# Performance work log

Measured on AMD Instinct MI355X. Metric: run time of the kernel, lower is better.

Reference implementation:

```python
import jax, jax.numpy as jnp
import numpy as np

N = 50000      # nodes
E = 800000     # edges (avg degree 16)
IN, HID, OUT = 256, 128, 64
K, ALPHA = 4, 0.0  # APPNPConv(k=4, alpha=0.0)


def setup_inputs() -> dict:
    key = jax.random.key(0)
    ks = jax.random.split(key, 5)
    features = jax.random.normal(ks[0], (N, IN), jnp.float32)
    src = jax.random.randint(ks[1], (E,), 0, N, jnp.int32)
    dst = jax.random.randint(ks[2], (E,), 0, N, jnp.int32)
    W1 = jax.random.normal(ks[3], (IN, HID), jnp.float32) / np.float32(np.sqrt(IN))
    b1 = jnp.zeros((HID,), jnp.float32)
    W3 = jax.random.normal(ks[4], (HID, OUT), jnp.float32) / np.float32(np.sqrt(HID))
    b3 = jnp.zeros((OUT,), jnp.float32)
    return dict(features=features, src=src, dst=dst, W1=W1, b1=b1, W3=W3, b3=b3)


def _sym_norms(src, dst, n):
    # D_out^{-1/2} for source side, D_in^{-1/2} for destination side (DGL norm='both')
    ones = jnp.ones((src.shape[0],), jnp.float32)
    deg_out = jax.ops.segment_sum(ones, src, num_segments=n)
    deg_in = jax.ops.segment_sum(ones, dst, num_segments=n)
    return jnp.clip(deg_out, 1.0) ** -0.5, jnp.clip(deg_in, 1.0) ** -0.5


def _prop(x, src, dst, norm_src, norm_dst):
    # x: [N, D]. Symmetric-normalized SpMM: D_in^{-1/2} A D_out^{-1/2} x
    msg = (x * norm_src[:, None])[src]                       # [E, D] gather
    agg = jax.ops.segment_sum(msg, dst, num_segments=x.shape[0])  # [N, D] scatter-add
    return agg * norm_dst[:, None]


def reference(features, src, dst, W1, b1, W3, b3):
    ns, nd = _sym_norms(src, dst, N)
    # GraphConv 1 (weight-first since in_dim > hidden_dim; math identical either way)
    h = _prop(features @ W1, src, dst, ns, nd) + b1
    # dropout is identity in eval mode (training=False)
    # APPNPConv: k=4 power-iteration steps with teleport alpha=0.0
    h0 = h
    for _ in range(K):
        h = (1.0 - ALPHA) * _prop(h, src, dst, ns, nd) + ALPHA * h0
    # GraphConv 3
    out = _prop(h @ W3, src, dst, ns, nd) + b3
    return out
```

## Files before the change

### kernel.cpp

```cpp
#include <hip/hip_runtime.h>
#include <math.h>

#define N_NODES 50000
#define N_EDGES 800000
#define DIN 256
#define DHID 128
#define DOUT 64
#define CSTRIDE 64
#define ZROW N_NODES
#define HBLOCKS 256
#define HCHUNK (N_EDGES / HBLOCKS)
#define HWORDS (N_NODES / 4)
#define SLICE ((size_t)(N_NODES + 1) * 16)
#define NGROUPS (N_NODES / 4)
#define PBLOCKS 49

#define SB_SENT 3125
#define SB_HS (SB_SENT + HBLOCKS)
#define SB_HD (SB_HS + HBLOCKS)
#define SB_TOT (SB_HD + 66)

__global__ void k_setup(const int* __restrict__ src, const int* __restrict__ dst,
                        unsigned int* __restrict__ pS, unsigned int* __restrict__ pD,
                        unsigned int* __restrict__ csr32,
                        const float* __restrict__ W1, const float* __restrict__ b1,
                        const float* __restrict__ W3,
                        float* __restrict__ W13, float* __restrict__ bb,
                        float* __restrict__ Y0, float* __restrict__ Y1) {
    __shared__ unsigned int h[HWORDS];
    int bx = blockIdx.x, t = threadIdx.x;
    if (bx < SB_SENT) {
        unsigned int v = (unsigned int)ZROW | ((unsigned int)ZROW << 16);
        uint2 o; o.x = v; o.y = v;
        ((uint2*)csr32)[bx * 256 + t] = o;
        return;
    }
    if (bx < SB_HD) {
        const int* idx = (bx < SB_HS) ? src : dst;
        unsigned int* outp = (bx < SB_HS) ? pS : pD;
        int hb = bx - ((bx < SB_HS) ? SB_SENT : SB_HS);
        for (int w = t; w < HWORDS; w += 256) h[w] = 0u;
        __syncthreads();
        int base = hb * HCHUNK;
        for (int i = t; i < HCHUNK; i += 256) {
            int s = idx[base + i];
            atomicAdd(&h[s >> 2], 1u << ((s & 3) << 3));
        }
        __syncthreads();
        outp += (size_t)hb * HWORDS;
        for (int w = t; w < HWORDS; w += 256) outp[w] = h[w];
        return;
    }
    int vb = bx - SB_HD;
    if (vb == 65) {
        if (t < 64) {
            int qq = t >> 4, c2 = t & 15;
            Y0[(size_t)qq * SLICE + ((size_t)ZROW << 4) + c2] = 0.f;
            Y1[(size_t)qq * SLICE + ((size_t)ZROW << 4) + c2] = 0.f;
        }
        return;
    }
    if (vb == 64) {
        if (t < DOUT) {
            float s = 0.f;
            for (int k = 0; k < DHID; ++k) s += b1[k] * W3[k * DOUT + t];
            bb[t] = s;
        }
        return;
    }
    int idx2 = vb * 256 + t;
    int i = idx2 >> 6, j = idx2 & 63;
    float s = 0.f;
    for (int k = 0; k < DHID; ++k) s += W1[i * DHID + k] * W3[k * DOUT + j];
    W13[idx2] = s;
}

__global__ void k_hpre(const unsigned int* __restrict__ pS,
                       const unsigned int* __restrict__ pD,
                       unsigned int* __restrict__ prefix,
                       int* __restrict__ deg_in,
                       float* __restrict__ ns, float* __restrict__ nd,
                       float* __restrict__ cc, int* __restrict__ dparts) {
    __shared__ int lh[65];
    int t = threadIdx.x;
    if (t < 65) lh[t] = 0;
    __syncthreads();
    int wid = blockIdx.x * 256 + t;
    if (wid < HWORDS) {
        unsigned int o0 = 0, o1 = 0, o2 = 0, o3 = 0;
#pragma unroll 4
        for (int b = 0; b < HBLOCKS; ++b) {
            unsigned int w = pS[(size_t)b * HWORDS + wid];
            o0 += w & 0xffu; o1 += (w >> 8) & 0xffu;
            o2 += (w >> 16) & 0xffu; o3 += w >> 24;
        }
        unsigned int run = 0;
        for (int b = 0; b < HBLOCKS; ++b) {
            unsigned int w = pD[(size_t)b * HWORDS + wid];
            prefix[(size_t)b * HWORDS + wid] = run;
            run += w;
        }
        unsigned int i0 = run & 0xffu, i1 = (run >> 8) & 0xffu;
        unsigned int i2 = (run >> 16) & 0xffu, i3 = run >> 24;
        int4 di; di.x = (int)i0; di.y = (int)i1; di.z = (int)i2; di.w = (int)i3;
        *(int4*)(deg_in + (wid << 2)) = di;

        unsigned int dov[4] = {o0, o1, o2, o3};
        unsigned int div_[4] = {i0, i1, i2, i3};
        float4 vns, vnd, vcc;
        float* pns = &vns.x; float* pnd = &vnd.x; float* pcc = &vcc.x;
#pragma unroll
        for (int q = 0; q < 4; ++q) {
            int bin = (int)div_[q]; if (bin > 64) bin = 64;
            atomicAdd(&lh[bin], 1);
            unsigned int a = dov[q] < 1u ? 1u : dov[q];
            unsigned int b = div_[q] < 1u ? 1u : div_[q];
            float fa = 1.0f / sqrtf((float)a);
            float fb = 1.0f / sqrtf((float)b);
            pns[q] = fa; pnd[q] = fb; pcc[q] = fa * fb;
        }
        *(float4*)(ns + (wid << 2)) = vns;
        *(float4*)(nd + (wid << 2)) = vnd;
        *(float4*)(cc + (wid << 2)) = vcc;
    }
    __syncthreads();
    if (t < 65) dparts[blockIdx.x * 65 + t] = lh[t];
}

__global__ void k_dscan(const int* __restrict__ dparts, int* __restrict__ offs) {
    __shared__ int colsum[65], binbase[65];
    int t = threadIdx.x;
    if (t < 65) {
        int s = 0;
        for (int b = 0; b < PBLOCKS; ++b) s += dparts[b * 65 + t];
        colsum[t] = s;
    }
    __syncthreads();
    if (t == 0) {
        int run = 0;
        for (int k = 64; k >= 0; --k) { binbase[k] = run; run += colsum[k]; }
    }
    __syncthreads();
    if (t < 65) {
        int run = binbase[t];
        for (int b = 0; b < PBLOCKS; ++b) { offs[b * 65 + t] = run; run += dparts[b * 65 + t]; }
    }
}

__global__ void k_dscatter(const int* __restrict__ deg_in, const int* __restrict__ offs,
                           const float* __restrict__ cc, const float* __restrict__ ns,
                           const float* __restrict__ nd,
                           int* __restrict__ perm, int* __restrict__ inv,
                           int* __restrict__ degP, float* __restrict__ ccP,
                           float* __restrict__ nsP, float* __restrict__ ndP) {
    __shared__ int off[65];
    int t = threadIdx.x;
    if (t < 65) off[t] = offs[blockIdx.x * 65 + t];
    __syncthreads();
    int wid = blockIdx.x * 256 + t;
    if (wid < HWORDS) {
        int4 d4 = *(const int4*)(deg_in + (wid << 2));
        int dd[4] = {d4.x, d4.y, d4.z, d4.w};
#pragma unroll
        for (int k = 0; k < 4; ++k) {
            int node = (wid << 2) + k;
            int bin = dd[k] > 64 ? 64 : dd[k];
            int slot = atomicAdd(&off[bin], 1);
            perm[slot] = node; inv[node] = slot;
            degP[slot] = dd[k];
            ccP[slot] = cc[node]; nsP[slot] = ns[node]; ndP[slot] = nd[node];
        }
    }
}

__global__ void k_fill(const int* __restrict__ src, const int* __restrict__ dst,
                       const unsigned int* __restrict__ prefix,
                       const int* __restrict__ inv,
                       unsigned short* __restrict__ csr) {
    __shared__ unsigned int h[HWORDS];
    int t = threadIdx.x;
    const unsigned int* prow = prefix + (size_t)blockIdx.x * HWORDS;
    for (int w = t; w < HWORDS; w += 256) h[w] = prow[w];
    __syncthreads();
    int base = blockIdx.x * HCHUNK;
    for (int i = t; i < HCHUNK; i += 256) {
        int s = src[base + i], d = dst[base + i];
        int sh = (d & 3) << 3;
        unsigned int old = atomicAdd(&h[d >> 2], 1u << sh);
        int slot = (int)((old >> sh) & 0xffu);
        csr[((size_t)inv[d] << 6) + slot] = (unsigned short)inv[s];
    }
}

__global__ void k_gemm(const float* __restrict__ X, const float* __restrict__ W13,
                       const float* __restrict__ ns, const int* __restrict__ inv,
                       float* __restrict__ Y) {
    __shared__ float As[16][68];
    __shared__ float Bs[16][64];
    int tid = threadIdx.x;
    int tx = tid & 15, ty = tid >> 4;
    int row0 = blockIdx.x * 64;
    float acc[4][4];
#pragma unroll
    for (int i = 0; i < 4; ++i)
#pragma unroll
        for (int j = 0; j < 4; ++j) acc[i][j] = 0.f;

    int lr = tid >> 2;
    int lk = (tid & 3) << 2;
    int arow = row0 + lr;
    if (arow > N_NODES - 1) arow = N_NODES - 1;

    for (int k0 = 0; k0 < DIN; k0 += 16) {
        float4 a = *(const float4*)(X + (size_t)arow * DIN + k0 + lk);
        As[lk + 0][lr] = a.x; As[lk + 1][lr] = a.y;
        As[lk + 2][lr] = a.z; As[lk + 3][lr] = a.w;
        float4 b = *(const float4*)(W13 + (size_t)(k0 + (tid >> 4)) * DOUT + ((tid & 15) << 2));
        *(float4*)&Bs[tid >> 4][(tid & 15) << 2] = b;
        __syncthreads();
#pragma unroll
        for (int k = 0; k < 16; ++k) {
            float4 av = *(const float4*)&As[k][ty << 2];
            float4 bv = *(const float4*)&Bs[k][tx << 2];
            float ar[4] = {av.x, av.y, av.z, av.w};
            float br[4] = {bv.x, bv.y, bv.z, bv.w};
#pragma unroll
            for (int i = 0; i < 4; ++i)
#pragma unroll
                for (int j = 0; j < 4; ++j) acc[i][j] += ar[i] * br[j];
        }
        __syncthreads();
    }
    int qq = tx >> 2;
    int co = (tx & 3) << 2;
#pragma unroll
    for (int i = 0; i < 4; ++i) {
        int row = row0 + (ty << 2) + i;
        if (row < N_NODES) {
            float nsr = ns[row];
            int prow = inv[row];
            float4 o;
            o.x = acc[i][0] * nsr; o.y = acc[i][1] * nsr;
            o.z = acc[i][2] * nsr; o.w = acc[i][3] * nsr;
            *(float4*)(Y + (size_t)qq * SLICE + ((size_t)prow << 4) + co) = o;
        }
    }
}


template <int MODE>
__launch_bounds__(256, 8)
__global__ void k_spmm(const float* __restrict__ xs, float* __restrict__ ys,
                       const unsigned short* __restrict__ csr,
                       const int* __restrict__ degP,
                       const float* __restrict__ ccP, const float* __restrict__ nsP,
                       const float* __restrict__ ndP,
                       const float* __restrict__ bb, const float* __restrict__ b3,
                       const int* __restrict__ perm) {
    __shared__ unsigned short rows[4][4][64];
    int wid  = threadIdx.x >> 6;
    int lane = threadIdx.x & 63;
    int q    = (blockIdx.x & 7) >> 1;
    int half = blockIdx.x & 1;
    int g    = (blockIdx.x >> 3) * 8 + wid * 2 + half;
    if (g >= NGROUPS) return;
    int node0 = g << 2;

    int nn = lane >> 4, sl = lane & 15;
    const uint2* crow = (const uint2*)(csr + ((size_t)(node0 + nn) << 6)) + sl;
    uint2 rv = *crow;
    *(uint2*)(&rows[wid][nn][sl << 2]) = rv;

    int n0u = __builtin_amdgcn_readfirstlane(node0);
    int m = (degP[n0u] + 7) & ~7;

    int n = lane >> 4, e = (lane >> 2) & 3, c4 = lane & 3;
    const unsigned short* rd = &rows[wid][n][e];
    const float* xq = xs + (size_t)q * SLICE + (c4 << 2);

    float ax = 0.f, ay = 0.f, az = 0.f, aw = 0.f;
#define LDV(T) const float4 v##T = *(const float4*)(xq + ((size_t)rd[4 * (T)] << 4))
#define ACCV(T) ax += v##T.x; ay += v##T.y; az += v##T.z; aw += v##T.w
    if (m <= 8) {
        LDV(0); LDV(1);
        ACCV(0); ACCV(1);
    } else if (m <= 16) {
        LDV(0); LDV(1); LDV(2); LDV(3);
        ACCV(0); ACCV(1); ACCV(2); ACCV(3);
    } else if (m <= 24) {
        LDV(0); LDV(1); LDV(2); LDV(3); LDV(4); LDV(5);
        ACCV(0); ACCV(1); ACCV(2); ACCV(3); ACCV(4); ACCV(5);
    } else if (m <= 32) {
        LDV(0); LDV(1); LDV(2); LDV(3); LDV(4); LDV(5); LDV(6); LDV(7);
        ACCV(0); ACCV(1); ACCV(2); ACCV(3); ACCV(4); ACCV(5); ACCV(6); ACCV(7);
    } else {
        for (int j = 0; j < m; j += 8) {
            const float4 a = *(const float4*)(xq + ((size_t)rd[j] << 4));
            const float4 b = *(const float4*)(xq + ((size_t)rd[j + 4] << 4));
            ax += a.x; ay += a.y; az += a.z; aw += a.w;
            ax += b.x; ay += b.y; az += b.z; aw += b.w;
        }
    }
#undef LDV
#undef ACCV
    ax += __shfl_xor(ax, 4);  ay += __shfl_xor(ay, 4);
    az += __shfl_xor(az, 4);  aw += __shfl_xor(aw, 4);
    ax += __shfl_xor(ax, 8);  ay += __shfl_xor(ay, 8);
    az += __shfl_xor(az, 8);  aw += __shfl_xor(aw, 8);

    int nodeL = node0 + n;
    int colq  = (q << 4) + (c4 << 2);
    float4 r;
    if (MODE == 0) {
        float cv = ccP[nodeL], nv = nsP[nodeL];
        float4 bv = *(const float4*)(bb + colq);
        r.x = cv * ax + nv * bv.x; r.y = cv * ay + nv * bv.y;
        r.z = cv * az + nv * bv.z; r.w = cv * aw + nv * bv.w;
    } else if (MODE == 1) {
        float cv = ccP[nodeL];
        r.x = cv * ax; r.y = cv * ay; r.z = cv * az; r.w = cv * aw;
    } else {
        float dv = ndP[nodeL];
        float4 bv = *(const float4*)(b3 + colq);
        r.x = dv * ax + bv.x; r.y = dv * ay + bv.y;
        r.z = dv * az + bv.z; r.w = dv * aw + bv.w;
    }
    if (e == 0) {
        if (MODE == 2) {
            int orow = perm[nodeL];
            *(float4*)(ys + ((size_t)orow << 6) + colq) = r;
        } else {
            *(float4*)(ys + (size_t)q * SLICE + ((size_t)nodeL << 4) + (c4 << 2)) = r;
        }
    }
}


extern "C" void kernel_launch(void* const* d_in, const int* in_sizes, int n_in,
                              void* d_out, int out_size, void* d_ws, size_t ws_size,
                              hipStream_t stream) {
    const float* X   = (const float*)d_in[0];
    const int*   src = (const int*)d_in[1];
    const int*   dst = (const int*)d_in[2];
    const float* W1  = (const float*)d_in[3];
    const float* b1  = (const float*)d_in[4];
    const float* W3  = (const float*)d_in[5];
    const float* b3  = (const float*)d_in[6];
    float* out = (float*)d_out;

    char* ws = (char*)d_ws;
    size_t off = 0;
    auto alloc = [&](size_t bytes) -> void* {
        void* p = ws + off;
        off = (off + bytes + 255) & ~(size_t)255;
        return p;
    };
    unsigned int*   pS     = (unsigned int*)alloc((size_t)HBLOCKS * HWORDS * 4);
    unsigned int*   pD     = (unsigned int*)alloc((size_t)HBLOCKS * HWORDS * 4);
    unsigned int*   pref   = (unsigned int*)alloc((size_t)HBLOCKS * HWORDS * 4);
    float*          Y0     = (float*)alloc(SLICE * 4 * 4);
    float*          Y1     = (float*)alloc(SLICE * 4 * 4);
    unsigned short* csr    = (unsigned short*)alloc((size_t)N_NODES * CSTRIDE * 2);
    int*            deg_in = (int*)alloc((size_t)N_NODES * 4);
    float*          ns     = (float*)alloc((size_t)N_NODES * 4);
    float*          nd     = (float*)alloc((size_t)N_NODES * 4);
    float*          cc     = (float*)alloc((size_t)N_NODES * 4);
    int*            perm   = (int*)alloc((size_t)N_NODES * 4);
    int*            inv    = (int*)alloc((size_t)N_NODES * 4);
    int*            degP   = (int*)alloc((size_t)N_NODES * 4);
    float*          ccP    = (float*)alloc((size_t)N_NODES * 4);
    float*          nsP    = (float*)alloc((size_t)N_NODES * 4);
    float*          ndP    = (float*)alloc((size_t)N_NODES * 4);
    int*            dparts = (int*)alloc((size_t)PBLOCKS * 65 * 4);
    int*            offs   = (int*)alloc((size_t)PBLOCKS * 65 * 4);
    float*          W13    = (float*)alloc((size_t)DIN * DOUT * 4);
    float*          bb     = (float*)alloc(DOUT * 4);

    const int sblk = 1563 * 8;

    k_setup<<<SB_TOT, 256, 0, stream>>>(src, dst, pS, pD, (unsigned int*)csr,
                                        W1, b1, W3, W13, bb, Y0, Y1);
    k_hpre<<<PBLOCKS, 256, 0, stream>>>(pS, pD, pref, deg_in, ns, nd, cc, dparts);
    k_dscan<<<1, 256, 0, stream>>>(dparts, offs);
    k_dscatter<<<PBLOCKS, 256, 0, stream>>>(deg_in, offs, cc, ns, nd,
                                            perm, inv, degP, ccP, nsP, ndP);
    k_fill<<<HBLOCKS, 256, 0, stream>>>(src, dst, pref, inv, csr);

    k_gemm<<<(N_NODES + 63) / 64, 256, 0, stream>>>(X, W13, ns, inv, Y0);

    k_spmm<0><<<sblk, 256, 0, stream>>>(Y0, Y1, csr, degP, ccP, nsP, ndP, bb, b3, perm);
    k_spmm<1><<<sblk, 256, 0, stream>>>(Y1, Y0, csr, degP, ccP, nsP, ndP, bb, b3, perm);
    k_spmm<1><<<sblk, 256, 0, stream>>>(Y0, Y1, csr, degP, ccP, nsP, ndP, bb, b3, perm);
    k_spmm<1><<<sblk, 256, 0, stream>>>(Y1, Y0, csr, degP, ccP, nsP, ndP, bb, b3, perm);
    k_spmm<1><<<sblk, 256, 0, stream>>>(Y0, Y1, csr, degP, ccP, nsP, ndP, bb, b3, perm);
    k_spmm<2><<<sblk, 256, 0, stream>>>(Y1, out, csr, degP, ccP, nsP, ndP, bb, b3, perm);
}
```

Measured before the change: 315.3 us.

## Split histogram prefix scan across four threads per word and transpose LDS row layout

```diff
diff --git a/kernel.cpp b/kernel.cpp
--- a/kernel.cpp
+++ b/kernel.cpp
@@ -13,7 +13,7 @@
 #define HWORDS (N_NODES / 4)
 #define SLICE ((size_t)(N_NODES + 1) * 16)
 #define NGROUPS (N_NODES / 4)
-#define PBLOCKS 49
+#define P2BLOCKS 196
 
 #define SB_SENT 3125
 #define SB_HS (SB_SENT + HBLOCKS)
@@ -81,47 +81,61 @@
                        int* __restrict__ deg_in,
                        float* __restrict__ ns, float* __restrict__ nd,
                        float* __restrict__ cc, int* __restrict__ dparts) {
+    __shared__ unsigned int sdw[64][4];
+    __shared__ unsigned int sow[64][4];
     __shared__ int lh[65];
     int t = threadIdx.x;
     if (t < 65) lh[t] = 0;
-    __syncthreads();
-    int wid = blockIdx.x * 256 + t;
-    if (wid < HWORDS) {
-        unsigned int o0 = 0, o1 = 0, o2 = 0, o3 = 0;
+    int col = t >> 2, sub = t & 3;
+    int wid = blockIdx.x * 64 + col;
+    bool act = wid < HWORDS;
+    unsigned int ps = 0, pd = 0;
+    if (act) {
+        int b0 = sub << 6;
 #pragma unroll 4
-        for (int b = 0; b < HBLOCKS; ++b) {
-            unsigned int w = pS[(size_t)b * HWORDS + wid];
-            o0 += w & 0xffu; o1 += (w >> 8) & 0xffu;
-            o2 += (w >> 16) & 0xffu; o3 += w >> 24;
-        }
-        unsigned int run = 0;
-        for (int b = 0; b < HBLOCKS; ++b) {
+        for (int b = b0; b < b0 + 64; ++b) {
+            ps += pS[(size_t)b * HWORDS + wid];
+            pd += pD[(size_t)b * HWORDS + wid];
+        }
+    }
+    sdw[col][sub] = pd;
+    sow[col][sub] = ps;
+    __syncthreads();
+    if (act) {
+        unsigned int base = 0;
+        for (int k = 0; k < sub; ++k) base += sdw[col][k];
+        int b0 = sub << 6;
+        unsigned int run = base;
+        for (int b = b0; b < b0 + 64; ++b) {
             unsigned int w = pD[(size_t)b * HWORDS + wid];
             prefix[(size_t)b * HWORDS + wid] = run;
             run += w;
         }
-        unsigned int i0 = run & 0xffu, i1 = (run >> 8) & 0xffu;
-        unsigned int i2 = (run >> 16) & 0xffu, i3 = run >> 24;
-        int4 di; di.x = (int)i0; di.y = (int)i1; di.z = (int)i2; di.w = (int)i3;
-        *(int4*)(deg_in + (wid << 2)) = di;
-
-        unsigned int dov[4] = {o0, o1, o2, o3};
-        unsigned int div_[4] = {i0, i1, i2, i3};
-        float4 vns, vnd, vcc;
-        float* pns = &vns.x; float* pnd = &vnd.x; float* pcc = &vcc.x;
-#pragma unroll
-        for (int q = 0; q < 4; ++q) {
-            int bin = (int)div_[q]; if (bin > 64) bin = 64;
-            atomicAdd(&lh[bin], 1);
-            unsigned int a = dov[q] < 1u ? 1u : dov[q];
-            unsigned int b = div_[q] < 1u ? 1u : div_[q];
-            float fa = 1.0f / sqrtf((float)a);
-            float fb = 1.0f / sqrtf((float)b);
-            pns[q] = fa; pnd[q] = fb; pcc[q] = fa * fb;
-        }
-        *(float4*)(ns + (wid << 2)) = vns;
-        *(float4*)(nd + (wid << 2)) = vnd;
-        *(float4*)(cc + (wid << 2)) = vcc;
+        if (sub == 0) {
+            unsigned int totd = sdw[col][0] + sdw[col][1] + sdw[col][2] + sdw[col][3];
+            unsigned int toto = sow[col][0] + sow[col][1] + sow[col][2] + sow[col][3];
+            unsigned int di[4] = {totd & 0xffu, (totd >> 8) & 0xffu,
+                                  (totd >> 16) & 0xffu, totd >> 24};
+            unsigned int dov[4] = {toto & 0xffu, (toto >> 8) & 0xffu,
+                                   (toto >> 16) & 0xffu, toto >> 24};
+            int4 dd; dd.x = (int)di[0]; dd.y = (int)di[1]; dd.z = (int)di[2]; dd.w = (int)di[3];
+            *(int4*)(deg_in + (wid << 2)) = dd;
+            float4 vns, vnd, vcc;
+            float* pns = &vns.x; float* pnd = &vnd.x; float* pcc = &vcc.x;
+#pragma unroll
+            for (int q = 0; q < 4; ++q) {
+                int bin = (int)di[q]; if (bin > 64) bin = 64;
+                atomicAdd(&lh[bin], 1);
+                unsigned int a = dov[q] < 1u ? 1u : dov[q];
+                unsigned int b = di[q] < 1u ? 1u : di[q];
+                float fa = 1.0f / sqrtf((float)a);
+                float fb = 1.0f / sqrtf((float)b);
+                pns[q] = fa; pnd[q] = fb; pcc[q] = fa * fb;
+            }
+            *(float4*)(ns + (wid << 2)) = vns;
+            *(float4*)(nd + (wid << 2)) = vnd;
+            *(float4*)(cc + (wid << 2)) = vcc;
+        }
     }
     __syncthreads();
     if (t < 65) dparts[blockIdx.x * 65 + t] = lh[t];
@@ -132,7 +146,7 @@
     int t = threadIdx.x;
     if (t < 65) {
         int s = 0;
-        for (int b = 0; b < PBLOCKS; ++b) s += dparts[b * 65 + t];
+        for (int b = 0; b < P2BLOCKS; ++b) s += dparts[b * 65 + t];
         colsum[t] = s;
     }
     __syncthreads();
@@ -143,7 +157,7 @@
     __syncthreads();
     if (t < 65) {
         int run = binbase[t];
-        for (int b = 0; b < PBLOCKS; ++b) { offs[b * 65 + t] = run; run += dparts[b * 65 + t]; }
+        for (int b = 0; b < P2BLOCKS; ++b) { offs[b * 65 + t] = run; run += dparts[b * 65 + t]; }
     }
 }
 
@@ -157,8 +171,8 @@
     int t = threadIdx.x;
     if (t < 65) off[t] = offs[blockIdx.x * 65 + t];
     __syncthreads();
-    int wid = blockIdx.x * 256 + t;
-    if (wid < HWORDS) {
+    int wid = blockIdx.x * 64 + t;
+    if (t < 64 && wid < HWORDS) {
         int4 d4 = *(const int4*)(deg_in + (wid << 2));
         int dd[4] = {d4.x, d4.y, d4.z, d4.w};
 #pragma unroll
@@ -257,7 +271,7 @@
                        const float* __restrict__ ndP,
                        const float* __restrict__ bb, const float* __restrict__ b3,
                        const int* __restrict__ perm) {
-    __shared__ unsigned short rows[4][4][64];
+    __shared__ unsigned short rows[4][256];
     int wid  = threadIdx.x >> 6;
     int lane = threadIdx.x & 63;
     int q    = (blockIdx.x & 7) >> 1;
@@ -269,17 +283,21 @@
     int nn = lane >> 4, sl = lane & 15;
     const uint2* crow = (const uint2*)(csr + ((size_t)(node0 + nn) << 6)) + sl;
     uint2 rv = *crow;
-    *(uint2*)(&rows[wid][nn][sl << 2]) = rv;
+    unsigned short* bp = &rows[wid][(sl << 4) + nn];
+    bp[0]  = (unsigned short)(rv.x & 0xffffu);
+    bp[4]  = (unsigned short)(rv.x >> 16);
+    bp[8]  = (unsigned short)(rv.y & 0xffffu);
+    bp[12] = (unsigned short)(rv.y >> 16);
 
     int n0u = __builtin_amdgcn_readfirstlane(node0);
     int m = (degP[n0u] + 7) & ~7;
 
     int n = lane >> 4, e = (lane >> 2) & 3, c4 = lane & 3;
-    const unsigned short* rd = &rows[wid][n][e];
+    const unsigned short* rd = &rows[wid][(e << 2) + n];
     const float* xq = xs + (size_t)q * SLICE + (c4 << 2);
 
     float ax = 0.f, ay = 0.f, az = 0.f, aw = 0.f;
-#define LDV(T) const float4 v##T = *(const float4*)(xq + ((size_t)rd[4 * (T)] << 4))
+#define LDV(T) const float4 v##T = *(const float4*)(xq + ((size_t)rd[16 * (T)] << 4))
 #define ACCV(T) ax += v##T.x; ay += v##T.y; az += v##T.z; aw += v##T.w
     if (m <= 8) {
         LDV(0); LDV(1);
@@ -294,9 +312,10 @@
         LDV(0); LDV(1); LDV(2); LDV(3); LDV(4); LDV(5); LDV(6); LDV(7);
         ACCV(0); ACCV(1); ACCV(2); ACCV(3); ACCV(4); ACCV(5); ACCV(6); ACCV(7);
     } else {
-        for (int j = 0; j < m; j += 8) {
-            const float4 a = *(const float4*)(xq + ((size_t)rd[j] << 4));
-            const float4 b = *(const float4*)(xq + ((size_t)rd[j + 4] << 4));
+        for (int j2 = 0; j2 < m; j2 += 8) {
+            int o = j2 << 2;
+            const float4 a = *(const float4*)(xq + ((size_t)rd[o] << 4));
+            const float4 b = *(const float4*)(xq + ((size_t)rd[o + 16] << 4));
             ax += a.x; ay += a.y; az += a.z; aw += a.w;
             ax += b.x; ay += b.y; az += b.z; aw += b.w;
         }
@@ -371,8 +390,8 @@
     float*          ccP    = (float*)alloc((size_t)N_NODES * 4);
     float*          nsP    = (float*)alloc((size_t)N_NODES * 4);
     float*          ndP    = (float*)alloc((size_t)N_NODES * 4);
-    int*            dparts = (int*)alloc((size_t)PBLOCKS * 65 * 4);
-    int*            offs   = (int*)alloc((size_t)PBLOCKS * 65 * 4);
+    int*            dparts = (int*)alloc((size_t)P2BLOCKS * 65 * 4);
+    int*            offs   = (int*)alloc((size_t)P2BLOCKS * 65 * 4);
     float*          W13    = (float*)alloc((size_t)DIN * DOUT * 4);
     float*          bb     = (float*)alloc(DOUT * 4);
 
@@ -380,10 +399,10 @@
 
     k_setup<<<SB_TOT, 256, 0, stream>>>(src, dst, pS, pD, (unsigned int*)csr,
                                         W1, b1, W3, W13, bb, Y0, Y1);
-    k_hpre<<<PBLOCKS, 256, 0, stream>>>(pS, pD, pref, deg_in, ns, nd, cc, dparts);
-    k_dscan<<<1, 256, 0, stream>>>(dparts, offs);
-    k_dscatter<<<PBLOCKS, 256, 0, stream>>>(deg_in, offs, cc, ns, nd,
-                                            perm, inv, degP, ccP, nsP, ndP);
+    k_hpre<<<P2BLOCKS, 256, 0, stream>>>(pS, pD, pref, deg_in, ns, nd, cc, dparts);
+    k_dscan<<<1, 128, 0, stream>>>(dparts, offs);
+    k_dscatter<<<P2BLOCKS, 128, 0, stream>>>(deg_in, offs, cc, ns, nd,
+                                             perm, inv, degP, ccP, nsP, ndP);
     k_fill<<<HBLOCKS, 256, 0, stream>>>(src, dst, pref, inv, csr);
 
     k_gemm<<<(N_NODES + 63) / 64, 256, 0, stream>>>(X, W13, ns, inv, Y0);
```

Result: faster. 305.3 us (-3.2%).
